# Performance work log

Measured on AMD Instinct MI355X. Metric: run time of the kernel, lower is better.

## Reference

```python
import jax, jax.numpy as jnp
import numpy as np

NUM_HEADS = 16
D_MODEL = 1024
B, T = 2, 2048


def setup_inputs() -> dict:
    key = jax.random.key(0)
    ks = jax.random.split(key, 5)
    s = 1.0 / np.sqrt(D_MODEL)
    return {
        "x": jax.random.normal(ks[0], (B, T, D_MODEL), dtype=jnp.float32),
        "Wq": jax.random.normal(ks[1], (D_MODEL, D_MODEL), dtype=jnp.float32) * s,
        "Wk": jax.random.normal(ks[2], (D_MODEL, D_MODEL), dtype=jnp.float32) * s,
        "Wv": jax.random.normal(ks[3], (D_MODEL, D_MODEL), dtype=jnp.float32) * s,
        "Wo": jax.random.normal(ks[4], (D_MODEL, D_MODEL), dtype=jnp.float32) * s,
    }


def reference(x, Wq, Wk, Wv, Wo):
    # x: [B, T, D]; W*: [D, D] (torch nn.Linear weight layout, y = x @ W.T)
    b, t, d = x.shape
    h = NUM_HEADS
    hd = d // h

    def split_heads(y):
        # [B, T, D] -> [B, H, T, hd]
        return y.reshape(b, t, h, hd).transpose(0, 2, 1, 3)

    q = split_heads(x @ Wq.T)
    k = split_heads(x @ Wk.T)
    v = split_heads(x @ Wv.T)

    # scale uses last dim AFTER head split: 1/sqrt(head_dim)
    scores = jnp.einsum("bhqd,bhkd->bhqk", q, k) / jnp.sqrt(jnp.asarray(hd, x.dtype))
    causal = jnp.tril(jnp.ones((t, t), dtype=bool))  # [T, T]
    scores = jnp.where(causal[None, None], scores, -jnp.inf)
    attn = jax.nn.softmax(scores, axis=-1)  # [B, H, T, T]

    out = jnp.einsum("bhqk,bhkd->bhqd", attn, v)  # [B, H, T, hd]
    out = out.transpose(0, 2, 1, 3).reshape(b, t, d)  # concat heads
    return out @ Wo.T
```

## Files before the change

kernel.cpp:

```cpp
#include <hip/hip_runtime.h>
#include <hip/hip_bf16.h>

#define T_SEQ 2048
#define DM    1024
#define MTOT  4096

typedef short v8s __attribute__((ext_vector_type(8)));
typedef float v4f __attribute__((ext_vector_type(4)));

__device__ __forceinline__ unsigned short f2bf(float f) {
  union { float f; unsigned int u; } x; x.f = f;
  return (unsigned short)((x.u + (((x.u >> 16) & 1u) + 0x7fffu)) >> 16);
}

__device__ __forceinline__ void gload16(const void* g, void* lds) {
  __builtin_amdgcn_global_load_lds(
      (const __attribute__((address_space(1))) unsigned int*)g,
      (__attribute__((address_space(3))) unsigned int*)lds, 16, 0, 0);
}

__global__ __launch_bounds__(256) void convert_all(
    const float* __restrict__ x,
    const float* __restrict__ Wq, const float* __restrict__ Wk,
    const float* __restrict__ Wv, const float* __restrict__ Wo,
    unsigned short* __restrict__ xb, unsigned short* __restrict__ wb)
{
  int i = blockIdx.x * 256 + threadIdx.x;
  const float4* src;
  ushort4* dst;
  int idx;
  if (i < (1 << 20)) {
    src = (const float4*)x; dst = (ushort4*)xb; idx = i;
  } else {
    int j = i - (1 << 20);
    int wsel = j >> 18;
    idx = j & ((1 << 18) - 1);
    const float* s = (wsel == 0) ? Wq : (wsel == 1) ? Wk : (wsel == 2) ? Wv : Wo;
    src = (const float4*)s;
    dst = (ushort4*)(wb + (size_t)wsel * DM * DM);
  }
  float4 v = src[idx];
  ushort4 o = { f2bf(v.x), f2bf(v.y), f2bf(v.z), f2bf(v.w) };
  dst[idx] = o;
}

__device__ __forceinline__ void gemm128_main(
    const unsigned short* __restrict__ A,
    const unsigned short* __restrict__ Bw,
    int m0, int n0,
    unsigned short* As, unsigned short* Bs,
    v4f acc[4][4])
{
  const int tid  = threadIdx.x;
  const int wv   = tid >> 6, l = tid & 63;
  const int lrow = l & 15, lq = l >> 4;
  const int wm = wv >> 1, wn = wv & 1;
  const int srow = l >> 3, sslot = l & 7;
  const int swz  = sslot ^ (srow & 7);

  const size_t aBase = (size_t)(m0 + wv * 8 + srow) * DM + swz * 8;
  const size_t bBase = (size_t)(n0 + wv * 8 + srow) * DM + swz * 8;

  for (int k0 = 0; k0 < DM; k0 += 64) {
    __syncthreads();
#pragma unroll
    for (int i = 0; i < 4; ++i) {
      gload16(A  + aBase + (size_t)i * 32 * DM + k0, As + i * 2048 + wv * 512);
      gload16(Bw + bBase + (size_t)i * 32 * DM + k0, Bs + i * 2048 + wv * 512);
    }
    __syncthreads();
#pragma unroll
    for (int kc = 0; kc < 2; ++kc) {
      const int aslot = ((kc << 2) | lq) ^ (lrow & 7);
      v8s af[4], bf[4];
#pragma unroll
      for (int mt = 0; mt < 4; ++mt)
        af[mt] = *(const v8s*)&As[(wm * 64 + mt * 16 + lrow) * 64 + aslot * 8];
#pragma unroll
      for (int nt = 0; nt < 4; ++nt)
        bf[nt] = *(const v8s*)&Bs[(wn * 64 + nt * 16 + lrow) * 64 + aslot * 8];
#pragma unroll
      for (int mt = 0; mt < 4; ++mt)
#pragma unroll
        for (int nt = 0; nt < 4; ++nt)
          acc[mt][nt] = __builtin_amdgcn_mfma_f32_16x16x32_bf16(
              af[mt], bf[nt], acc[mt][nt], 0, 0, 0);
    }
  }
}

__global__ __launch_bounds__(256) void qkv_gemm128(
    const unsigned short* __restrict__ xb,
    const unsigned short* __restrict__ wb,
    unsigned short* __restrict__ Qw, unsigned short* __restrict__ Kw,
    unsigned short* __restrict__ Vtw)
{
  __shared__ unsigned short smem[2 * 128 * 64];
  unsigned short* As = smem;
  unsigned short* Bs = smem + 8192;
  const int z = blockIdx.z;
  const unsigned short* W = wb + (size_t)z * DM * DM;
  const int m0 = blockIdx.x * 128, n0 = blockIdx.y * 128;

  v4f acc[4][4];
#pragma unroll
  for (int mt = 0; mt < 4; ++mt)
#pragma unroll
    for (int nt = 0; nt < 4; ++nt) acc[mt][nt] = (v4f){0.f, 0.f, 0.f, 0.f};

  gemm128_main(xb, W, m0, n0, As, Bs, acc);

  const int tid = threadIdx.x;
  const int wv = tid >> 6, l = tid & 63;
  const int lrow = l & 15, lq = l >> 4;
  const int wm = wv >> 1, wn = wv & 1;

  if (z < 2) {
    unsigned short* Y = z ? Kw : Qw;
#pragma unroll
    for (int mt = 0; mt < 4; ++mt)
#pragma unroll
      for (int nt = 0; nt < 4; ++nt)
#pragma unroll
        for (int r = 0; r < 4; ++r) {
          int row = m0 + wm * 64 + mt * 16 + lq * 4 + r;
          int col = n0 + wn * 64 + nt * 16 + lrow;
          Y[(size_t)row * DM + col] = f2bf(acc[mt][nt][r]);
        }
  } else {
    __syncthreads();
#pragma unroll
    for (int mt = 0; mt < 4; ++mt)
#pragma unroll
      for (int nt = 0; nt < 4; ++nt)
#pragma unroll
        for (int r = 0; r < 4; ++r) {
          int trow = wm * 64 + mt * 16 + lq * 4 + r;
          int col  = wn * 64 + nt * 16 + lrow;
          int ch = col >> 3;
          int slot = (ch & 8) | ((ch & 7) ^ (trow & 7));
          smem[trow * 128 + slot * 8 + (col & 7)] = f2bf(acc[mt][nt][r]);
        }
    __syncthreads();
    const int d128 = tid & 127;
    const int halfsel = tid >> 7;
    const int bb = m0 >> 11;
    const int tblk = (m0 & 2047) >> 7;
    const int bh = bb * 16 + ((n0 + d128) >> 6);
    const int dh = d128 & 63;
    unsigned short* dst = Vtw + (((size_t)bh * 16 + tblk) * 64 + dh) * 128;
    const int ch = d128 >> 3, e7 = d128 & 7;
#pragma unroll
    for (int j = 0; j < 8; ++j) {
      int tchunk = j * 2 + halfsel;
      unsigned short vals[8];
#pragma unroll
      for (int e = 0; e < 8; ++e) {
        int tr = tchunk * 8 + e;
        int slot = (ch & 8) | ((ch & 7) ^ (tr & 7));
        vals[e] = smem[tr * 128 + slot * 8 + e7];
      }
      *(v8s*)(dst + tchunk * 8) = *(const v8s*)vals;
    }
  }
}

__global__ __launch_bounds__(256) void oproj_gemm128(
    const unsigned short* __restrict__ AO,
    const unsigned short* __restrict__ Wob,
    float* __restrict__ Y)
{
  __shared__ unsigned short smem[2 * 128 * 64];
  unsigned short* As = smem;
  unsigned short* Bs = smem + 8192;
  const int m0 = blockIdx.x * 128, n0 = blockIdx.y * 128;

  v4f acc[4][4];
#pragma unroll
  for (int mt = 0; mt < 4; ++mt)
#pragma unroll
    for (int nt = 0; nt < 4; ++nt) acc[mt][nt] = (v4f){0.f, 0.f, 0.f, 0.f};

  gemm128_main(AO, Wob, m0, n0, As, Bs, acc);

  const int tid = threadIdx.x;
  const int wv = tid >> 6, l = tid & 63;
  const int lrow = l & 15, lq = l >> 4;
  const int wm = wv >> 1, wn = wv & 1;
#pragma unroll
  for (int mt = 0; mt < 4; ++mt)
#pragma unroll
    for (int nt = 0; nt < 4; ++nt)
#pragma unroll
      for (int r = 0; r < 4; ++r) {
        int row = m0 + wm * 64 + mt * 16 + lq * 4 + r;
        int col = n0 + wn * 64 + nt * 16 + lrow;
        Y[(size_t)row * DM + col] = acc[mt][nt][r];
      }
}

__global__ __launch_bounds__(256) void attn3(
    const unsigned short* __restrict__ Q,
    const unsigned short* __restrict__ K,
    const unsigned short* __restrict__ Vt,
    unsigned short* __restrict__ O)
{
  __shared__ unsigned short Ks[128 * 64];
  __shared__ unsigned short Vts[64 * 128];
  __shared__ unsigned short Ps[64 * 128];

  const int tid  = threadIdx.x;
  const int wave = tid >> 6;
  const int lane = tid & 63;
  const int lrow = lane & 15;
  const int lq   = lane >> 4;
  const int gid  = blockIdx.x;
  const int qt   = 31 - (gid >> 5);
  const int bh   = gid & 31;
  const int b = bh >> 4, h = bh & 15;

  const int qrow = qt * 64 + wave * 16 + lrow;
  const unsigned short* qp = Q + ((size_t)(b * T_SEQ + qrow)) * DM + h * 64;
  v8s qf[2] = { *(const v8s*)(qp + lq * 8), *(const v8s*)(qp + 32 + lq * 8) };

  v4f oacc[4];
#pragma unroll
  for (int nt = 0; nt < 4; ++nt) oacc[nt] = (v4f){0.f, 0.f, 0.f, 0.f};
  float psum[4] = {0.f, 0.f, 0.f, 0.f};

  const int nkt = (qt >> 1) + 1;

  const int kchunk = (lane & 7) ^ ((lane >> 3) & 7);
  const unsigned short* kg =
      K + ((size_t)(b * T_SEQ) + wave * 8 + (lane >> 3)) * DM + h * 64 + kchunk * 8;
  unsigned short* kdst = Ks + (wave * 8) * 64;
  const int vd = wave * 4 + (lane >> 4);
  const int vslot = lane & 15;
  const int vchunk = (vslot & 8) | ((vslot & 7) ^ (vd & 7));
  const unsigned short* vg =
      Vt + (((size_t)bh * 16) * 64 + vd) * 128 + vchunk * 8;
  unsigned short* vdst = Vts + (wave * 4) * 128;

  for (int kt = 0; kt < nkt; ++kt) {
    __syncthreads();
#pragma unroll
    for (int i = 0; i < 4; ++i)
      gload16(kg + ((size_t)kt * 128 + i * 32) * DM, kdst + i * 32 * 64);
#pragma unroll
    for (int i = 0; i < 4; ++i)
      gload16(vg + ((size_t)kt * 64 + i * 16) * 128, vdst + i * 16 * 128);
    __syncthreads();

    v4f s[8];
#pragma unroll
    for (int nt = 0; nt < 8; ++nt) {
      v4f a = {0.f, 0.f, 0.f, 0.f};
#pragma unroll
      for (int kc = 0; kc < 2; ++kc) {
        int slot = (kc * 4 + lq) ^ (lrow & 7);
        v8s bfr = *(const v8s*)&Ks[(nt * 16 + lrow) * 64 + slot * 8];
        a = __builtin_amdgcn_mfma_f32_16x16x32_bf16(qf[kc], bfr, a, 0, 0, 0);
      }
      s[nt] = a;
    }

    const bool last = (kt == nkt - 1);
    if (last) {
#pragma unroll
      for (int nt = 0; nt < 8; ++nt)
#pragma unroll
        for (int r = 0; r < 4; ++r) {
          float p = exp2f(fmaf(s[nt][r], 0.18033688f, -23.0831206f));
          if (kt * 128 + nt * 16 + lrow > qt * 64 + wave * 16 + lq * 4 + r) p = 0.f;
          psum[r] += p;
          unsigned int bits = __float_as_uint(p);
          int ch = nt * 2 + (lrow >> 3);
          int slot = (ch & 8) | ((ch & 7) ^ ((lq * 4 + r) & 7));
          Ps[(wave * 16 + lq * 4 + r) * 128 + slot * 8 + (lrow & 7)] =
              (unsigned short)((bits + 0x8000u) >> 16);
        }
    } else {
#pragma unroll
      for (int nt = 0; nt < 8; ++nt)
#pragma unroll
        for (int r = 0; r < 4; ++r) {
          float p = exp2f(fmaf(s[nt][r], 0.18033688f, -23.0831206f));
          psum[r] += p;
          unsigned int bits = __float_as_uint(p);
          int ch = nt * 2 + (lrow >> 3);
          int slot = (ch & 8) | ((ch & 7) ^ ((lq * 4 + r) & 7));
          Ps[(wave * 16 + lq * 4 + r) * 128 + slot * 8 + (lrow & 7)] =
              (unsigned short)((bits + 0x8000u) >> 16);
        }
    }

    v8s pf[4];
#pragma unroll
    for (int kc = 0; kc < 4; ++kc) {
      int ch = kc * 4 + lq;
      int slot = (ch & 8) | ((ch & 7) ^ (lrow & 7));
      pf[kc] = *(const v8s*)&Ps[(wave * 16 + lrow) * 128 + slot * 8];
    }

#pragma unroll
    for (int nt = 0; nt < 4; ++nt)
#pragma unroll
      for (int kc = 0; kc < 4; ++kc) {
        int ch = kc * 4 + lq;
        int slot = (ch & 8) | ((ch & 7) ^ (lrow & 7));
        v8s vb = *(const v8s*)&Vts[(nt * 16 + lrow) * 128 + slot * 8];
        oacc[nt] = __builtin_amdgcn_mfma_f32_16x16x32_bf16(pf[kc], vb, oacc[nt], 0, 0, 0);
      }
  }

#pragma unroll
  for (int r = 0; r < 4; ++r) {
    float ps = psum[r];
#pragma unroll
    for (int off = 1; off < 16; off <<= 1) ps += __shfl_xor(ps, off);
    psum[r] = ps;
  }
#pragma unroll
  for (int nt = 0; nt < 4; ++nt)
#pragma unroll
    for (int r = 0; r < 4; ++r) {
      int trow = qt * 64 + wave * 16 + lq * 4 + r;
      int col  = h * 64 + nt * 16 + lrow;
      O[((size_t)(b * T_SEQ + trow)) * DM + col] = f2bf(oacc[nt][r] / psum[r]);
    }
}

extern "C" void kernel_launch(void* const* d_in, const int* in_sizes, int n_in,
                              void* d_out, int out_size, void* d_ws, size_t ws_size,
                              hipStream_t stream) {
  const float* x  = (const float*)d_in[0];
  const float* Wq = (const float*)d_in[1];
  const float* Wk = (const float*)d_in[2];
  const float* Wv = (const float*)d_in[3];
  const float* Wo = (const float*)d_in[4];
  float* out = (float*)d_out;

  unsigned short* xb  = (unsigned short*)d_ws;
  unsigned short* wb  = xb + (size_t)MTOT * DM;
  unsigned short* Qw  = wb + (size_t)4 * DM * DM;
  unsigned short* Kw  = Qw + (size_t)MTOT * DM;
  unsigned short* Vtw = Kw + (size_t)MTOT * DM;
  unsigned short* AO  = xb;

  convert_all<<<8192, 256, 0, stream>>>(x, Wq, Wk, Wv, Wo, xb, wb);
  qkv_gemm128<<<dim3(32, 8, 3), 256, 0, stream>>>(xb, wb, Qw, Kw, Vtw);
  attn3<<<1024, 256, 0, stream>>>(Qw, Kw, Vtw, AO);
  oproj_gemm128<<<dim3(32, 8), 256, 0, stream>>>(AO, wb + (size_t)3 * DM * DM, out);
}
```

Before: 181.6 us.

## Fuse Q/K/V projections into one GEMM and enlarge attention query tile

The three QKV projections now run in one kernel that loads each x tile once and multiplies it against all three weight tiles, holding three accumulator sets. The attention kernel moves from 64 to 128 query rows per block, so each K/V tile load is reused by twice as many rows. Block order is changed to interleave long and short causal rows. This cuts redundant global loads but raises register pressure (192 accumulator floats in the QKV GEMM) and LDS use, and halves the number of blocks, which may lower occupancy and parallelism.

```diff
diff --git a/kernel.cpp b/kernel.cpp
--- a/kernel.cpp
+++ b/kernel.cpp
@@ -44,19 +44,30 @@
   dst[idx] = o;
 }
 
-__device__ __forceinline__ void gemm128_main(
-    const unsigned short* __restrict__ A,
-    const unsigned short* __restrict__ Bw,
-    int m0, int n0,
-    unsigned short* As, unsigned short* Bs,
-    v4f acc[4][4])
+__global__ __launch_bounds__(256) void qkv_fused(
+    const unsigned short* __restrict__ xb,
+    const unsigned short* __restrict__ wb,
+    unsigned short* __restrict__ Qw, unsigned short* __restrict__ Kw,
+    unsigned short* __restrict__ Vtw)
 {
+  __shared__ unsigned short smem[4 * 128 * 64];
+  unsigned short* As = smem;
+
   const int tid  = threadIdx.x;
   const int wv   = tid >> 6, l = tid & 63;
   const int lrow = l & 15, lq = l >> 4;
   const int wm = wv >> 1, wn = wv & 1;
   const int srow = l >> 3, sslot = l & 7;
   const int swz  = sslot ^ (srow & 7);
+  const int m0 = blockIdx.x * 128, n0 = blockIdx.y * 128;
+
+  v4f acc[3][4][4];
+#pragma unroll
+  for (int z = 0; z < 3; ++z)
+#pragma unroll
+    for (int mt = 0; mt < 4; ++mt)
+#pragma unroll
+      for (int nt = 0; nt < 4; ++nt) acc[z][mt][nt] = (v4f){0.f, 0.f, 0.f, 0.f};
 
   const size_t aBase = (size_t)(m0 + wv * 8 + srow) * DM + swz * 8;
   const size_t bBase = (size_t)(n0 + wv * 8 + srow) * DM + swz * 8;
@@ -64,58 +75,41 @@
   for (int k0 = 0; k0 < DM; k0 += 64) {
     __syncthreads();
 #pragma unroll
-    for (int i = 0; i < 4; ++i) {
-      gload16(A  + aBase + (size_t)i * 32 * DM + k0, As + i * 2048 + wv * 512);
-      gload16(Bw + bBase + (size_t)i * 32 * DM + k0, Bs + i * 2048 + wv * 512);
-    }
+    for (int i = 0; i < 4; ++i)
+      gload16(xb + aBase + (size_t)i * 32 * DM + k0, As + i * 2048 + wv * 512);
+#pragma unroll
+    for (int z = 0; z < 3; ++z)
+#pragma unroll
+      for (int i = 0; i < 4; ++i)
+        gload16(wb + (size_t)z * DM * DM + bBase + (size_t)i * 32 * DM + k0,
+                smem + (1 + z) * 8192 + i * 2048 + wv * 512);
     __syncthreads();
 #pragma unroll
     for (int kc = 0; kc < 2; ++kc) {
       const int aslot = ((kc << 2) | lq) ^ (lrow & 7);
-      v8s af[4], bf[4];
+      v8s af[4];
 #pragma unroll
       for (int mt = 0; mt < 4; ++mt)
         af[mt] = *(const v8s*)&As[(wm * 64 + mt * 16 + lrow) * 64 + aslot * 8];
 #pragma unroll
-      for (int nt = 0; nt < 4; ++nt)
-        bf[nt] = *(const v8s*)&Bs[(wn * 64 + nt * 16 + lrow) * 64 + aslot * 8];
-#pragma unroll
-      for (int mt = 0; mt < 4; ++mt)
+      for (int z = 0; z < 3; ++z) {
+        const unsigned short* Bz = smem + (1 + z) * 8192;
+        v8s bf[4];
 #pragma unroll
         for (int nt = 0; nt < 4; ++nt)
-          acc[mt][nt] = __builtin_amdgcn_mfma_f32_16x16x32_bf16(
-              af[mt], bf[nt], acc[mt][nt], 0, 0, 0);
-    }
-  }
-}
-
-__global__ __launch_bounds__(256) void qkv_gemm128(
-    const unsigned short* __restrict__ xb,
-    const unsigned short* __restrict__ wb,
-    unsigned short* __restrict__ Qw, unsigned short* __restrict__ Kw,
-    unsigned short* __restrict__ Vtw)
-{
-  __shared__ unsigned short smem[2 * 128 * 64];
-  unsigned short* As = smem;
-  unsigned short* Bs = smem + 8192;
-  const int z = blockIdx.z;
-  const unsigned short* W = wb + (size_t)z * DM * DM;
-  const int m0 = blockIdx.x * 128, n0 = blockIdx.y * 128;
-
-  v4f acc[4][4];
-#pragma unroll
-  for (int mt = 0; mt < 4; ++mt)
-#pragma unroll
-    for (int nt = 0; nt < 4; ++nt) acc[mt][nt] = (v4f){0.f, 0.f, 0.f, 0.f};
-
-  gemm128_main(xb, W, m0, n0, As, Bs, acc);
-
-  const int tid = threadIdx.x;
-  const int wv = tid >> 6, l = tid & 63;
-  const int lrow = l & 15, lq = l >> 4;
-  const int wm = wv >> 1, wn = wv & 1;
-
-  if (z < 2) {
+          bf[nt] = *(const v8s*)&Bz[(wn * 64 + nt * 16 + lrow) * 64 + aslot * 8];
+#pragma unroll
+        for (int mt = 0; mt < 4; ++mt)
+#pragma unroll
+          for (int nt = 0; nt < 4; ++nt)
+            acc[z][mt][nt] = __builtin_amdgcn_mfma_f32_16x16x32_bf16(
+                af[mt], bf[nt], acc[z][mt][nt], 0, 0, 0);
+      }
+    }
+  }
+
+#pragma unroll
+  for (int z = 0; z < 2; ++z) {
     unsigned short* Y = z ? Kw : Qw;
 #pragma unroll
     for (int mt = 0; mt < 4; ++mt)
@@ -125,23 +119,25 @@
         for (int r = 0; r < 4; ++r) {
           int row = m0 + wm * 64 + mt * 16 + lq * 4 + r;
           int col = n0 + wn * 64 + nt * 16 + lrow;
-          Y[(size_t)row * DM + col] = f2bf(acc[mt][nt][r]);
+          Y[(size_t)row * DM + col] = f2bf(acc[z][mt][nt][r]);
         }
-  } else {
-    __syncthreads();
-#pragma unroll
-    for (int mt = 0; mt < 4; ++mt)
-#pragma unroll
-      for (int nt = 0; nt < 4; ++nt)
-#pragma unroll
-        for (int r = 0; r < 4; ++r) {
-          int trow = wm * 64 + mt * 16 + lq * 4 + r;
-          int col  = wn * 64 + nt * 16 + lrow;
-          int ch = col >> 3;
-          int slot = (ch & 8) | ((ch & 7) ^ (trow & 7));
-          smem[trow * 128 + slot * 8 + (col & 7)] = f2bf(acc[mt][nt][r]);
-        }
-    __syncthreads();
+  }
+
+  __syncthreads();
+#pragma unroll
+  for (int mt = 0; mt < 4; ++mt)
+#pragma unroll
+    for (int nt = 0; nt < 4; ++nt)
+#pragma unroll
+      for (int r = 0; r < 4; ++r) {
+        int trow = wm * 64 + mt * 16 + lq * 4 + r;
+        int col  = wn * 64 + nt * 16 + lrow;
+        int ch = col >> 3;
+        int slot = (ch & 8) | ((ch & 7) ^ (trow & 7));
+        smem[trow * 128 + slot * 8 + (col & 7)] = f2bf(acc[2][mt][nt][r]);
+      }
+  __syncthreads();
+  {
     const int d128 = tid & 127;
     const int halfsel = tid >> 7;
     const int bb = m0 >> 11;
@@ -173,20 +169,49 @@
   __shared__ unsigned short smem[2 * 128 * 64];
   unsigned short* As = smem;
   unsigned short* Bs = smem + 8192;
-  const int m0 = blockIdx.x * 128, n0 = blockIdx.y * 128;
-
-  v4f acc[4][4];
-#pragma unroll
-  for (int mt = 0; mt < 4; ++mt)
-#pragma unroll
-    for (int nt = 0; nt < 4; ++nt) acc[mt][nt] = (v4f){0.f, 0.f, 0.f, 0.f};
-
-  gemm128_main(AO, Wob, m0, n0, As, Bs, acc);
-
-  const int tid = threadIdx.x;
-  const int wv = tid >> 6, l = tid & 63;
+  const int tid  = threadIdx.x;
+  const int wv   = tid >> 6, l = tid & 63;
   const int lrow = l & 15, lq = l >> 4;
   const int wm = wv >> 1, wn = wv & 1;
+  const int srow = l >> 3, sslot = l & 7;
+  const int swz  = sslot ^ (srow & 7);
+  const int m0 = blockIdx.x * 128, n0 = blockIdx.y * 128;
+
+  v4f acc[4][4];
+#pragma unroll
+  for (int mt = 0; mt < 4; ++mt)
+#pragma unroll
+    for (int nt = 0; nt < 4; ++nt) acc[mt][nt] = (v4f){0.f, 0.f, 0.f, 0.f};
+
+  const size_t aBase = (size_t)(m0 + wv * 8 + srow) * DM + swz * 8;
+  const size_t bBase = (size_t)(n0 + wv * 8 + srow) * DM + swz * 8;
+
+  for (int k0 = 0; k0 < DM; k0 += 64) {
+    __syncthreads();
+#pragma unroll
+    for (int i = 0; i < 4; ++i) {
+      gload16(AO  + aBase + (size_t)i * 32 * DM + k0, As + i * 2048 + wv * 512);
+      gload16(Wob + bBase + (size_t)i * 32 * DM + k0, Bs + i * 2048 + wv * 512);
+    }
+    __syncthreads();
+#pragma unroll
+    for (int kc = 0; kc < 2; ++kc) {
+      const int aslot = ((kc << 2) | lq) ^ (lrow & 7);
+      v8s af[4], bf[4];
+#pragma unroll
+      for (int mt = 0; mt < 4; ++mt)
+        af[mt] = *(const v8s*)&As[(wm * 64 + mt * 16 + lrow) * 64 + aslot * 8];
+#pragma unroll
+      for (int nt = 0; nt < 4; ++nt)
+        bf[nt] = *(const v8s*)&Bs[(wn * 64 + nt * 16 + lrow) * 64 + aslot * 8];
+#pragma unroll
+      for (int mt = 0; mt < 4; ++mt)
+#pragma unroll
+        for (int nt = 0; nt < 4; ++nt)
+          acc[mt][nt] = __builtin_amdgcn_mfma_f32_16x16x32_bf16(
+              af[mt], bf[nt], acc[mt][nt], 0, 0, 0);
+    }
+  }
 #pragma unroll
   for (int mt = 0; mt < 4; ++mt)
 #pragma unroll
@@ -199,7 +224,7 @@
       }
 }
 
-__global__ __launch_bounds__(256) void attn3(
+__global__ __launch_bounds__(256) void attn4(
     const unsigned short* __restrict__ Q,
     const unsigned short* __restrict__ K,
     const unsigned short* __restrict__ Vt,
@@ -207,7 +232,7 @@
 {
   __shared__ unsigned short Ks[128 * 64];
   __shared__ unsigned short Vts[64 * 128];
-  __shared__ unsigned short Ps[64 * 128];
+  __shared__ unsigned short Ps[128 * 128];
 
   const int tid  = threadIdx.x;
   const int wave = tid >> 6;
@@ -215,20 +240,27 @@
   const int lrow = lane & 15;
   const int lq   = lane >> 4;
   const int gid  = blockIdx.x;
-  const int qt   = 31 - (gid >> 5);
+  const int qt   = (gid < 256) ? (15 - (gid >> 5)) : ((gid >> 5) - 8);
   const int bh   = gid & 31;
   const int b = bh >> 4, h = bh & 15;
 
-  const int qrow = qt * 64 + wave * 16 + lrow;
-  const unsigned short* qp = Q + ((size_t)(b * T_SEQ + qrow)) * DM + h * 64;
-  v8s qf[2] = { *(const v8s*)(qp + lq * 8), *(const v8s*)(qp + 32 + lq * 8) };
-
-  v4f oacc[4];
-#pragma unroll
-  for (int nt = 0; nt < 4; ++nt) oacc[nt] = (v4f){0.f, 0.f, 0.f, 0.f};
-  float psum[4] = {0.f, 0.f, 0.f, 0.f};
-
-  const int nkt = (qt >> 1) + 1;
+  v8s qf[2][2];
+#pragma unroll
+  for (int mt = 0; mt < 2; ++mt) {
+    const unsigned short* qp =
+        Q + ((size_t)(b * T_SEQ + qt * 128 + wave * 32 + mt * 16 + lrow)) * DM + h * 64;
+    qf[mt][0] = *(const v8s*)(qp + lq * 8);
+    qf[mt][1] = *(const v8s*)(qp + 32 + lq * 8);
+  }
+
+  v4f oacc[2][4];
+#pragma unroll
+  for (int mt = 0; mt < 2; ++mt)
+#pragma unroll
+    for (int nt = 0; nt < 4; ++nt) oacc[mt][nt] = (v4f){0.f, 0.f, 0.f, 0.f};
+  float psum[2][4] = {{0.f,0.f,0.f,0.f},{0.f,0.f,0.f,0.f}};
+
+  const int nkt = qt + 1;
 
   const int kchunk = (lane & 7) ^ ((lane >> 3) & 7);
   const unsigned short* kg =
@@ -238,7 +270,7 @@
   const int vslot = lane & 15;
   const int vchunk = (vslot & 8) | ((vslot & 7) ^ (vd & 7));
   const unsigned short* vg =
-      Vt + (((size_t)bh * 16) * 64 + vd) * 128 + vchunk * 8;
+      Vt + ((size_t)bh * 1024 + vd) * 128 + vchunk * 8;
   unsigned short* vdst = Vts + (wave * 4) * 128;
 
   for (int kt = 0; kt < nkt; ++kt) {
@@ -248,86 +280,83 @@
       gload16(kg + ((size_t)kt * 128 + i * 32) * DM, kdst + i * 32 * 64);
 #pragma unroll
     for (int i = 0; i < 4; ++i)
-      gload16(vg + ((size_t)kt * 64 + i * 16) * 128, vdst + i * 16 * 128);
-    __syncthreads();
-
-    v4f s[8];
-#pragma unroll
-    for (int nt = 0; nt < 8; ++nt) {
-      v4f a = {0.f, 0.f, 0.f, 0.f};
-#pragma unroll
-      for (int kc = 0; kc < 2; ++kc) {
-        int slot = (kc * 4 + lq) ^ (lrow & 7);
-        v8s bfr = *(const v8s*)&Ks[(nt * 16 + lrow) * 64 + slot * 8];
-        a = __builtin_amdgcn_mfma_f32_16x16x32_bf16(qf[kc], bfr, a, 0, 0, 0);
-      }
-      s[nt] = a;
-    }
-
-    const bool last = (kt == nkt - 1);
-    if (last) {
+      gload16(vg + (size_t)kt * 8192 + i * 2048, vdst + i * 16 * 128);
+    __syncthreads();
+
+    v4f s[2][8];
+#pragma unroll
+    for (int mt = 0; mt < 2; ++mt)
+#pragma unroll
+      for (int nt = 0; nt < 8; ++nt) {
+        v4f a = {0.f, 0.f, 0.f, 0.f};
+#pragma unroll
+        for (int kc = 0; kc < 2; ++kc) {
+          int slot = (kc * 4 + lq) ^ (lrow & 7);
+          v8s bfr = *(const v8s*)&Ks[(nt * 16 + lrow) * 64 + slot * 8];
+          a = __builtin_amdgcn_mfma_f32_16x16x32_bf16(qf[mt][kc], bfr, a, 0, 0, 0);
+        }
+        s[mt][nt] = a;
+      }
+
+    const bool last = (kt == qt);
+#pragma unroll
+    for (int mt = 0; mt < 2; ++mt)
 #pragma unroll
       for (int nt = 0; nt < 8; ++nt)
 #pragma unroll
         for (int r = 0; r < 4; ++r) {
-          float p = exp2f(fmaf(s[nt][r], 0.18033688f, -23.0831206f));
-          if (kt * 128 + nt * 16 + lrow > qt * 64 + wave * 16 + lq * 4 + r) p = 0.f;
-          psum[r] += p;
+          float p = exp2f(fmaf(s[mt][nt][r], 0.18033688f, -23.0831206f));
+          if (last && (nt * 16 + lrow > wave * 32 + mt * 16 + lq * 4 + r)) p = 0.f;
+          psum[mt][r] += p;
           unsigned int bits = __float_as_uint(p);
+          int row = wave * 32 + mt * 16 + lq * 4 + r;
           int ch = nt * 2 + (lrow >> 3);
-          int slot = (ch & 8) | ((ch & 7) ^ ((lq * 4 + r) & 7));
-          Ps[(wave * 16 + lq * 4 + r) * 128 + slot * 8 + (lrow & 7)] =
+          int slot = (ch & 8) | ((ch & 7) ^ (row & 7));
+          Ps[row * 128 + slot * 8 + (lrow & 7)] =
               (unsigned short)((bits + 0x8000u) >> 16);
         }
-    } else {
-#pragma unroll
-      for (int nt = 0; nt < 8; ++nt)
-#pragma unroll
-        for (int r = 0; r < 4; ++r) {
-          float p = exp2f(fmaf(s[nt][r], 0.18033688f, -23.0831206f));
-          psum[r] += p;
-          unsigned int bits = __float_as_uint(p);
-          int ch = nt * 2 + (lrow >> 3);
-          int slot = (ch & 8) | ((ch & 7) ^ ((lq * 4 + r) & 7));
-          Ps[(wave * 16 + lq * 4 + r) * 128 + slot * 8 + (lrow & 7)] =
-              (unsigned short)((bits + 0x8000u) >> 16);
-        }
-    }
-
-    v8s pf[4];
-#pragma unroll
-    for (int kc = 0; kc < 4; ++kc) {
-      int ch = kc * 4 + lq;
-      int slot = (ch & 8) | ((ch & 7) ^ (lrow & 7));
-      pf[kc] = *(const v8s*)&Ps[(wave * 16 + lrow) * 128 + slot * 8];
-    }
-
-#pragma unroll
-    for (int nt = 0; nt < 4; ++nt)
+
+#pragma unroll
+    for (int mt = 0; mt < 2; ++mt) {
+      v8s pf[4];
 #pragma unroll
       for (int kc = 0; kc < 4; ++kc) {
         int ch = kc * 4 + lq;
         int slot = (ch & 8) | ((ch & 7) ^ (lrow & 7));
-        v8s vb = *(const v8s*)&Vts[(nt * 16 + lrow) * 128 + slot * 8];
-        oacc[nt] = __builtin_amdgcn_mfma_f32_16x16x32_bf16(pf[kc], vb, oacc[nt], 0, 0, 0);
-      }
-  }
-
-#pragma unroll
-  for (int r = 0; r < 4; ++r) {
-    float ps = psum[r];
-#pragma unroll
-    for (int off = 1; off < 16; off <<= 1) ps += __shfl_xor(ps, off);
-    psum[r] = ps;
-  }
-#pragma unroll
-  for (int nt = 0; nt < 4; ++nt)
+        pf[kc] = *(const v8s*)&Ps[(wave * 32 + mt * 16 + lrow) * 128 + slot * 8];
+      }
+#pragma unroll
+      for (int nt = 0; nt < 4; ++nt)
+#pragma unroll
+        for (int kc = 0; kc < 4; ++kc) {
+          int ch = kc * 4 + lq;
+          int slot = (ch & 8) | ((ch & 7) ^ (lrow & 7));
+          v8s vb = *(const v8s*)&Vts[(nt * 16 + lrow) * 128 + slot * 8];
+          oacc[mt][nt] = __builtin_amdgcn_mfma_f32_16x16x32_bf16(
+              pf[kc], vb, oacc[mt][nt], 0, 0, 0);
+        }
+    }
+  }
+
+#pragma unroll
+  for (int mt = 0; mt < 2; ++mt)
 #pragma unroll
     for (int r = 0; r < 4; ++r) {
-      int trow = qt * 64 + wave * 16 + lq * 4 + r;
-      int col  = h * 64 + nt * 16 + lrow;
-      O[((size_t)(b * T_SEQ + trow)) * DM + col] = f2bf(oacc[nt][r] / psum[r]);
-    }
+      float ps = psum[mt][r];
+#pragma unroll
+      for (int off = 1; off < 16; off <<= 1) ps += __shfl_xor(ps, off);
+      psum[mt][r] = ps;
+    }
+#pragma unroll
+  for (int mt = 0; mt < 2; ++mt)
+#pragma unroll
+    for (int nt = 0; nt < 4; ++nt)
+#pragma unroll
+      for (int r = 0; r < 4; ++r) {
+        int trow = qt * 128 + wave * 32 + mt * 16 + lq * 4 + r;
+        int col  = h * 64 + nt * 16 + lrow;
+        O[((size_t)(b * T_SEQ + trow)) * DM + col] = f2bf(oacc[mt][nt][r] / psum[mt][r]);
+      }
 }
 
 extern "C" void kernel_launch(void* const* d_in, const int* in_sizes, int n_in,
@@ -348,7 +377,7 @@
   unsigned short* AO  = xb;
 
   convert_all<<<8192, 256, 0, stream>>>(x, Wq, Wk, Wv, Wo, xb, wb);
-  qkv_gemm128<<<dim3(32, 8, 3), 256, 0, stream>>>(xb, wb, Qw, Kw, Vtw);
-  attn3<<<1024, 256, 0, stream>>>(Qw, Kw, Vtw, AO);
+  qkv_fused<<<dim3(32, 8), 256, 0, stream>>>(xb, wb, Qw, Kw, Vtw);
+  attn4<<<512, 256, 0, stream>>>(Qw, Kw, Vtw, AO);
   oproj_gemm128<<<dim3(32, 8), 256, 0, stream>>>(AO, wb + (size_t)3 * DM * DM, out);
 }
```

After: 201.5 us. +11.0%, slower.

## Fuse Q/K/V projections into one kernel sharing A tile; shrink oproj tile

Applied to the files above, without the earlier changes.

The QKV projection now runs as a single kernel. Each block loads one 128x64 tile of x and multiplies it against 64-column slices of all three weight matrices, so the x tile is reused three times instead of being reloaded per z-slice. The V output is transposed through shared memory with a simpler 64-wide swizzle. The output projection moves to 64x128 tiles, giving 512 blocks instead of 256 to fill more CUs. The trade-off is more accumulator registers and more shared memory in the QKV kernel, which may lower occupancy.

```diff
diff --git a/kernel.cpp b/kernel.cpp
--- a/kernel.cpp
+++ b/kernel.cpp
@@ -44,156 +44,181 @@
   dst[idx] = o;
 }
 
-__device__ __forceinline__ void gemm128_main(
-    const unsigned short* __restrict__ A,
-    const unsigned short* __restrict__ Bw,
-    int m0, int n0,
-    unsigned short* As, unsigned short* Bs,
-    v4f acc[4][4])
-{
-  const int tid  = threadIdx.x;
-  const int wv   = tid >> 6, l = tid & 63;
-  const int lrow = l & 15, lq = l >> 4;
-  const int wm = wv >> 1, wn = wv & 1;
-  const int srow = l >> 3, sslot = l & 7;
-  const int swz  = sslot ^ (srow & 7);
-
-  const size_t aBase = (size_t)(m0 + wv * 8 + srow) * DM + swz * 8;
-  const size_t bBase = (size_t)(n0 + wv * 8 + srow) * DM + swz * 8;
-
-  for (int k0 = 0; k0 < DM; k0 += 64) {
-    __syncthreads();
-#pragma unroll
-    for (int i = 0; i < 4; ++i) {
-      gload16(A  + aBase + (size_t)i * 32 * DM + k0, As + i * 2048 + wv * 512);
-      gload16(Bw + bBase + (size_t)i * 32 * DM + k0, Bs + i * 2048 + wv * 512);
-    }
-    __syncthreads();
-#pragma unroll
-    for (int kc = 0; kc < 2; ++kc) {
-      const int aslot = ((kc << 2) | lq) ^ (lrow & 7);
-      v8s af[4], bf[4];
-#pragma unroll
-      for (int mt = 0; mt < 4; ++mt)
-        af[mt] = *(const v8s*)&As[(wm * 64 + mt * 16 + lrow) * 64 + aslot * 8];
-#pragma unroll
-      for (int nt = 0; nt < 4; ++nt)
-        bf[nt] = *(const v8s*)&Bs[(wn * 64 + nt * 16 + lrow) * 64 + aslot * 8];
-#pragma unroll
-      for (int mt = 0; mt < 4; ++mt)
-#pragma unroll
-        for (int nt = 0; nt < 4; ++nt)
-          acc[mt][nt] = __builtin_amdgcn_mfma_f32_16x16x32_bf16(
-              af[mt], bf[nt], acc[mt][nt], 0, 0, 0);
-    }
-  }
-}
-
-__global__ __launch_bounds__(256) void qkv_gemm128(
+__global__ __launch_bounds__(256) void qkv_fused2(
     const unsigned short* __restrict__ xb,
     const unsigned short* __restrict__ wb,
     unsigned short* __restrict__ Qw, unsigned short* __restrict__ Kw,
     unsigned short* __restrict__ Vtw)
 {
-  __shared__ unsigned short smem[2 * 128 * 64];
+  __shared__ unsigned short smem[20480];
   unsigned short* As = smem;
-  unsigned short* Bs = smem + 8192;
-  const int z = blockIdx.z;
-  const unsigned short* W = wb + (size_t)z * DM * DM;
-  const int m0 = blockIdx.x * 128, n0 = blockIdx.y * 128;
-
-  v4f acc[4][4];
-#pragma unroll
-  for (int mt = 0; mt < 4; ++mt)
-#pragma unroll
-    for (int nt = 0; nt < 4; ++nt) acc[mt][nt] = (v4f){0.f, 0.f, 0.f, 0.f};
-
-  gemm128_main(xb, W, m0, n0, As, Bs, acc);
-
-  const int tid = threadIdx.x;
-  const int wv = tid >> 6, l = tid & 63;
+
+  const int tid  = threadIdx.x;
+  const int wv   = tid >> 6, l = tid & 63;
   const int lrow = l & 15, lq = l >> 4;
-  const int wm = wv >> 1, wn = wv & 1;
-
-  if (z < 2) {
+  const int wm = wv >> 1;
+  const int wn = wv & 1;
+  const int srow = l >> 3, sslot = l & 7;
+  const int swz  = sslot ^ (srow & 7);
+  const int m0 = blockIdx.x * 128, n0 = blockIdx.y * 64;
+
+  v4f acc[3][4][2];
+#pragma unroll
+  for (int z = 0; z < 3; ++z)
+#pragma unroll
+    for (int mt = 0; mt < 4; ++mt)
+#pragma unroll
+      for (int nt = 0; nt < 2; ++nt) acc[z][mt][nt] = (v4f){0.f, 0.f, 0.f, 0.f};
+
+  const size_t aBase = (size_t)(m0 + wv * 32 + srow) * DM + swz * 8;
+  const size_t bBase = (size_t)(n0 + wv * 16 + srow) * DM + swz * 8;
+
+  for (int k0 = 0; k0 < DM; k0 += 64) {
+    __syncthreads();
+#pragma unroll
+    for (int i = 0; i < 4; ++i)
+      gload16(xb + aBase + (size_t)i * 8 * DM + k0, As + (wv * 32 + i * 8) * 64);
+#pragma unroll
+    for (int z = 0; z < 3; ++z)
+#pragma unroll
+      for (int i = 0; i < 2; ++i)
+        gload16(wb + (size_t)z * DM * DM + bBase + (size_t)i * 8 * DM + k0,
+                smem + 8192 + z * 4096 + (wv * 16 + i * 8) * 64);
+    __syncthreads();
+#pragma unroll
+    for (int kc = 0; kc < 2; ++kc) {
+      const int aslot = ((kc << 2) | lq) ^ (lrow & 7);
+      v8s af[4];
+#pragma unroll
+      for (int mt = 0; mt < 4; ++mt)
+        af[mt] = *(const v8s*)&As[(wm * 64 + mt * 16 + lrow) * 64 + aslot * 8];
+#pragma unroll
+      for (int z = 0; z < 3; ++z) {
+        const unsigned short* Bz = smem + 8192 + z * 4096;
+        v8s bf[2];
+#pragma unroll
+        for (int nt = 0; nt < 2; ++nt)
+          bf[nt] = *(const v8s*)&Bz[(wn * 32 + nt * 16 + lrow) * 64 + aslot * 8];
+#pragma unroll
+        for (int mt = 0; mt < 4; ++mt)
+#pragma unroll
+          for (int nt = 0; nt < 2; ++nt)
+            acc[z][mt][nt] = __builtin_amdgcn_mfma_f32_16x16x32_bf16(
+                af[mt], bf[nt], acc[z][mt][nt], 0, 0, 0);
+      }
+    }
+  }
+
+#pragma unroll
+  for (int z = 0; z < 2; ++z) {
     unsigned short* Y = z ? Kw : Qw;
 #pragma unroll
     for (int mt = 0; mt < 4; ++mt)
 #pragma unroll
-      for (int nt = 0; nt < 4; ++nt)
+      for (int nt = 0; nt < 2; ++nt)
 #pragma unroll
         for (int r = 0; r < 4; ++r) {
           int row = m0 + wm * 64 + mt * 16 + lq * 4 + r;
-          int col = n0 + wn * 64 + nt * 16 + lrow;
-          Y[(size_t)row * DM + col] = f2bf(acc[mt][nt][r]);
+          int col = n0 + wn * 32 + nt * 16 + lrow;
+          Y[(size_t)row * DM + col] = f2bf(acc[z][mt][nt][r]);
         }
-  } else {
-    __syncthreads();
-#pragma unroll
-    for (int mt = 0; mt < 4; ++mt)
-#pragma unroll
-      for (int nt = 0; nt < 4; ++nt)
-#pragma unroll
-        for (int r = 0; r < 4; ++r) {
-          int trow = wm * 64 + mt * 16 + lq * 4 + r;
-          int col  = wn * 64 + nt * 16 + lrow;
-          int ch = col >> 3;
-          int slot = (ch & 8) | ((ch & 7) ^ (trow & 7));
-          smem[trow * 128 + slot * 8 + (col & 7)] = f2bf(acc[mt][nt][r]);
-        }
-    __syncthreads();
-    const int d128 = tid & 127;
-    const int halfsel = tid >> 7;
-    const int bb = m0 >> 11;
+  }
+
+  __syncthreads();
+#pragma unroll
+  for (int mt = 0; mt < 4; ++mt)
+#pragma unroll
+    for (int nt = 0; nt < 2; ++nt)
+#pragma unroll
+      for (int r = 0; r < 4; ++r) {
+        int trow = wm * 64 + mt * 16 + lq * 4 + r;
+        int col  = wn * 32 + nt * 16 + lrow;
+        int slot = (col >> 3) ^ (trow & 7);
+        smem[trow * 64 + slot * 8 + (col & 7)] = f2bf(acc[2][mt][nt][r]);
+      }
+  __syncthreads();
+  {
+    const int d = tid & 63;
+    const int quarter = tid >> 6;
+    const int b = m0 >> 11;
     const int tblk = (m0 & 2047) >> 7;
-    const int bh = bb * 16 + ((n0 + d128) >> 6);
-    const int dh = d128 & 63;
-    unsigned short* dst = Vtw + (((size_t)bh * 16 + tblk) * 64 + dh) * 128;
-    const int ch = d128 >> 3, e7 = d128 & 7;
-#pragma unroll
-    for (int j = 0; j < 8; ++j) {
-      int tchunk = j * 2 + halfsel;
+    const int h = n0 >> 6;
+    const int bh = b * 16 + h;
+    unsigned short* dst = Vtw + (((size_t)bh * 16 + tblk) * 64 + d) * 128;
+    const int ch = d >> 3, e7 = d & 7;
+#pragma unroll
+    for (int j = 0; j < 4; ++j) {
+      int tbase = quarter * 32 + j * 8;
       unsigned short vals[8];
 #pragma unroll
-      for (int e = 0; e < 8; ++e) {
-        int tr = tchunk * 8 + e;
-        int slot = (ch & 8) | ((ch & 7) ^ (tr & 7));
-        vals[e] = smem[tr * 128 + slot * 8 + e7];
-      }
-      *(v8s*)(dst + tchunk * 8) = *(const v8s*)vals;
-    }
-  }
-}
-
-__global__ __launch_bounds__(256) void oproj_gemm128(
+      for (int e = 0; e < 8; ++e)
+        vals[e] = smem[(tbase + e) * 64 + (ch ^ e) * 8 + e7];
+      *(v8s*)(dst + tbase) = *(const v8s*)vals;
+    }
+  }
+}
+
+__global__ __launch_bounds__(256) void oproj_gemm2(
     const unsigned short* __restrict__ AO,
     const unsigned short* __restrict__ Wob,
     float* __restrict__ Y)
 {
-  __shared__ unsigned short smem[2 * 128 * 64];
+  __shared__ unsigned short smem[12288];
   unsigned short* As = smem;
-  unsigned short* Bs = smem + 8192;
-  const int m0 = blockIdx.x * 128, n0 = blockIdx.y * 128;
-
-  v4f acc[4][4];
-#pragma unroll
-  for (int mt = 0; mt < 4; ++mt)
+  unsigned short* Bs = smem + 4096;
+
+  const int tid  = threadIdx.x;
+  const int wv   = tid >> 6, l = tid & 63;
+  const int lrow = l & 15, lq = l >> 4;
+  const int wm = wv >> 1;
+  const int wn = wv & 1;
+  const int srow = l >> 3, sslot = l & 7;
+  const int swz  = sslot ^ (srow & 7);
+  const int m0 = blockIdx.x * 64, n0 = blockIdx.y * 128;
+
+  v4f acc[2][4];
+#pragma unroll
+  for (int mt = 0; mt < 2; ++mt)
 #pragma unroll
     for (int nt = 0; nt < 4; ++nt) acc[mt][nt] = (v4f){0.f, 0.f, 0.f, 0.f};
 
-  gemm128_main(AO, Wob, m0, n0, As, Bs, acc);
-
-  const int tid = threadIdx.x;
-  const int wv = tid >> 6, l = tid & 63;
-  const int lrow = l & 15, lq = l >> 4;
-  const int wm = wv >> 1, wn = wv & 1;
-#pragma unroll
-  for (int mt = 0; mt < 4; ++mt)
+  const size_t aBase = (size_t)(m0 + wv * 16 + srow) * DM + swz * 8;
+  const size_t bBase = (size_t)(n0 + wv * 32 + srow) * DM + swz * 8;
+
+  for (int k0 = 0; k0 < DM; k0 += 64) {
+    __syncthreads();
+#pragma unroll
+    for (int i = 0; i < 2; ++i)
+      gload16(AO + aBase + (size_t)i * 8 * DM + k0, As + (wv * 16 + i * 8) * 64);
+#pragma unroll
+    for (int i = 0; i < 4; ++i)
+      gload16(Wob + bBase + (size_t)i * 8 * DM + k0, Bs + (wv * 32 + i * 8) * 64);
+    __syncthreads();
+#pragma unroll
+    for (int kc = 0; kc < 2; ++kc) {
+      const int aslot = ((kc << 2) | lq) ^ (lrow & 7);
+      v8s af[2], bf[4];
+#pragma unroll
+      for (int mt = 0; mt < 2; ++mt)
+        af[mt] = *(const v8s*)&As[(wm * 32 + mt * 16 + lrow) * 64 + aslot * 8];
+#pragma unroll
+      for (int nt = 0; nt < 4; ++nt)
+        bf[nt] = *(const v8s*)&Bs[(wn * 64 + nt * 16 + lrow) * 64 + aslot * 8];
+#pragma unroll
+      for (int mt = 0; mt < 2; ++mt)
+#pragma unroll
+        for (int nt = 0; nt < 4; ++nt)
+          acc[mt][nt] = __builtin_amdgcn_mfma_f32_16x16x32_bf16(
+              af[mt], bf[nt], acc[mt][nt], 0, 0, 0);
+    }
+  }
+#pragma unroll
+  for (int mt = 0; mt < 2; ++mt)
 #pragma unroll
     for (int nt = 0; nt < 4; ++nt)
 #pragma unroll
       for (int r = 0; r < 4; ++r) {
-        int row = m0 + wm * 64 + mt * 16 + lq * 4 + r;
+        int row = m0 + wm * 32 + mt * 16 + lq * 4 + r;
         int col = n0 + wn * 64 + nt * 16 + lrow;
         Y[(size_t)row * DM + col] = acc[mt][nt][r];
       }
@@ -348,7 +373,7 @@
   unsigned short* AO  = xb;
 
   convert_all<<<8192, 256, 0, stream>>>(x, Wq, Wk, Wv, Wo, xb, wb);
-  qkv_gemm128<<<dim3(32, 8, 3), 256, 0, stream>>>(xb, wb, Qw, Kw, Vtw);
+  qkv_fused2<<<dim3(32, 16), 256, 0, stream>>>(xb, wb, Qw, Kw, Vtw);
   attn3<<<1024, 256, 0, stream>>>(Qw, Kw, Vtw, AO);
-  oproj_gemm128<<<dim3(32, 8), 256, 0, stream>>>(AO, wb + (size_t)3 * DM * DM, out);
-}
+  oproj_gemm2<<<dim3(64, 8), 256, 0, stream>>>(AO, wb + (size_t)3 * DM * DM, out);
+}
```

New measurement: 172.6 us. 5.0% less time.
